# Performance work log

Measured on AMD Instinct MI355X. Metric: run time of the kernel, lower is better.

The kernel has to match this reference:

```python
import jax, jax.numpy as jnp
import numpy as np

ITEM_NUM = 100000
H = 128          # hidden_size
L_PROTO = 500    # number of prototypes
K = 4            # top-k prototypes
SEQ = 50         # max_seq_length
B = 1024
TAO = 0.1
LAMBDA = 0.1
EPS = 1e-5


def layer_norm(x, g, b):
    mu = jnp.mean(x, axis=-1, keepdims=True)
    var = jnp.mean((x - mu) ** 2, axis=-1, keepdims=True)
    return (x - mu) * jax.lax.rsqrt(var + EPS) * g + b


def setup_inputs() -> dict:
    key = jax.random.key(0)
    ks = jax.random.split(key, 12)
    std = 0.02
    item_emb = jax.random.normal(ks[0], (ITEM_NUM, H), jnp.float32) * std
    item_emb = item_emb.at[0].set(0.0)  # padding_idx=0
    pos_emb = jax.random.normal(ks[1], (SEQ + 1, H), jnp.float32) * std
    pos_emb = pos_emb.at[0].set(0.0)    # padding_idx=0 (never hit when len==SEQ)
    proto = jax.random.normal(ks[2], (L_PROTO, H), jnp.float32) * std
    w1 = jax.random.normal(ks[3], (H, H), jnp.float32) * std
    w2 = jax.random.normal(ks[4], (H, 1), jnp.float32) * std
    w3 = jax.random.normal(ks[5], (H, H), jnp.float32) * std
    w4 = jax.random.normal(ks[6], (H, H), jnp.float32) * std
    w5 = jax.random.normal(ks[7], (H, K), jnp.float32) * std
    w6 = jax.random.normal(ks[8], (H, H), jnp.float32) * std
    w7 = jax.random.normal(ks[9], (H, 1), jnp.float32) * std
    seq = jax.random.randint(ks[10], (B, SEQ), 0, ITEM_NUM, dtype=jnp.int64)
    g = jnp.ones((H,), jnp.float32)
    b = jnp.zeros((H,), jnp.float32)
    return {
        'item_emb': item_emb, 'pos_emb': pos_emb, 'proto': proto,
        'w1': w1, 'w2': w2, 'w3': w3, 'w4': w4, 'w5': w5, 'w6': w6, 'w7': w7,
        'ln1_g': g, 'ln1_b': b, 'ln2_g': g, 'ln2_b': b,
        'ln3_g': g, 'ln3_b': b, 'ln4_g': g, 'ln4_b': b,
        'seq': seq,
    }


def reference(item_emb, pos_emb, proto, w1, w2, w3, w4, w5, w6, w7,
              ln1_g, ln1_b, ln2_g, ln2_b, ln3_g, ln3_b, ln4_g, ln4_b, seq):
    mask = (seq != 0).astype(jnp.float32)            # [B,S]
    ie = item_emb[seq]                               # [B,S,H]

    # self-attentive virtual concept vector
    sa_score = jnp.squeeze(jnp.tanh(ie @ w1) @ w2, -1)   # [B,S]
    sa_score = sa_score - (1.0 - mask) * 10000.0
    alpha = jax.nn.softmax(sa_score, axis=-1)
    vcv = jnp.einsum('bs,bsh->bh', alpha, ie)            # [B,H]

    # prototype routing: top-k by score
    s = vcv @ proto.T                                    # [B,L]
    chosen_s, rank = jax.lax.top_k(s, K)                 # [B,K]
    chosen_proto = proto[rank]                           # [B,K,H]
    chosen_proto = jax.nn.sigmoid(chosen_s)[..., None] * chosen_proto

    # item->prototype assignment
    p_kt_score = jnp.einsum('bsh,bkh->bsk',
                            layer_norm(ie @ w3, ln1_g, ln1_b),
                            layer_norm(chosen_proto, ln2_g, ln2_b))
    p_kt = jax.nn.softmax(p_kt_score, axis=-1) * mask[:, :, None]  # [B,S,K]

    # positional embedding (positions SEQ..1)
    position = SEQ - jnp.arange(SEQ)                     # [S]
    emb = pos_emb[position][None, :, :] + ie             # [B,S,H]

    a_k_score = jnp.swapaxes(jnp.tanh(emb @ w4) @ w5, 1, 2)   # [B,K,S]
    a_k = jax.nn.softmax(a_k_score, axis=-1) * mask[:, None, :]
    a_k = jnp.swapaxes(a_k, 1, 2)                        # [B,S,K]

    p = p_kt * a_k
    interesting = layer_norm(jnp.einsum('bsk,bsh->bkh', p, emb), ln3_g, ln3_b)  # [B,K,H]

    xu = jnp.einsum('bsk,bkh->bsh', p_kt, chosen_proto)  # [B,S,H]
    c_score = jnp.squeeze(jnp.tanh(xu @ w6) @ w7, -1) - (1.0 - mask) * 10000.0
    c_w = jax.nn.softmax(c_score, axis=-1)               # [B,S]
    c_apt = layer_norm(jnp.einsum('bs,bsh->bh', c_w, xu), ln4_g, ln4_b)  # [B,H]

    e_score = jnp.einsum('bh,bkh->bk', c_apt, interesting)
    e = jax.nn.softmax(e_score / TAO, axis=-1)
    final = jnp.einsum('bk,bkh->bh', e, interesting)     # [B,H]
    scores = final @ item_emb.T                          # [B,ITEM_NUM]

    # prototype covariance regularizer
    centered = proto - jnp.mean(proto, axis=0, keepdims=True)
    M = (centered @ centered.T) / H
    Lc = (jnp.linalg.norm(M) - jnp.linalg.norm(jnp.diag(M))) * 0.5
    return scores, LAMBDA * Lc
```

## Files before the change

kernel.cpp:

```cpp
#include <hip/hip_runtime.h>
#include <hip/hip_bf16.h>

#define H 128
#define H2 132
#define SQL 50
#define LPROTO 500
#define KTOP 4
#define BQ 1024
#define ITEMS 100000

typedef __attribute__((ext_vector_type(8))) short bf16x8;
typedef __attribute__((ext_vector_type(4))) float f32x4;

__device__ __forceinline__ float wsum(float v){
#pragma unroll
  for (int o = 32; o; o >>= 1) v += __shfl_xor(v, o, 64);
  return v;
}
__device__ __forceinline__ float wmax(float v){
#pragma unroll
  for (int o = 32; o; o >>= 1) v = fmaxf(v, __shfl_xor(v, o, 64));
  return v;
}
__device__ __forceinline__ unsigned short f2bf(float x){
  unsigned int u = __builtin_bit_cast(unsigned int, x);
  unsigned int r = u + 0x7fffu + ((u >> 16) & 1u);
  return (unsigned short)(r >> 16);
}
__device__ __forceinline__ float bf2f(unsigned short h){
  unsigned int u = ((unsigned int)h) << 16;
  return __builtin_bit_cast(float, u);
}

__device__ __forceinline__ void mm_mfma(const float (*src)[H2], float (*dst)[H2],
                                        const unsigned short* __restrict__ wt_hi,
                                        const unsigned short* __restrict__ wt_lo,
                                        int lane, int wave)
{
  const int r15 = lane & 15;
  const int g   = lane >> 4;
  const int kof = g * 8;
  const int row = wave * 16 + r15;
  const int srow = (row < SQL) ? row : 0;

  bf16x8 ah[4], al[4];
#pragma unroll
  for (int ks = 0; ks < 4; ks++){
    const float* p = &src[srow][ks * 32 + kof];
    float4 x0 = *reinterpret_cast<const float4*>(p);
    float4 x1 = *reinterpret_cast<const float4*>(p + 4);
    float xs[8] = {x0.x, x0.y, x0.z, x0.w, x1.x, x1.y, x1.z, x1.w};
    bf16x8 h, l;
#pragma unroll
    for (int e = 0; e < 8; e++){
      unsigned short hb = f2bf(xs[e]);
      float rem = xs[e] - bf2f(hb);
      h[e] = (short)hb;
      l[e] = (short)f2bf(rem);
    }
    ah[ks] = h; al[ks] = l;
  }

  f32x4 acc[8];
#pragma unroll
  for (int j = 0; j < 8; j++) acc[j] = (f32x4){0.f, 0.f, 0.f, 0.f};

#pragma unroll
  for (int j = 0; j < 8; j++){
    const unsigned short* bp = wt_hi + (j * 16 + r15) * H + kof;
    const unsigned short* lp = wt_lo + (j * 16 + r15) * H + kof;
    f32x4 a = acc[j];
#pragma unroll
    for (int ks = 0; ks < 4; ks++){
      bf16x8 bh = *reinterpret_cast<const bf16x8*>(bp + ks * 32);
      bf16x8 bl = *reinterpret_cast<const bf16x8*>(lp + ks * 32);
      a = __builtin_amdgcn_mfma_f32_16x16x32_bf16(ah[ks], bh, a, 0, 0, 0);
      a = __builtin_amdgcn_mfma_f32_16x16x32_bf16(al[ks], bh, a, 0, 0, 0);
      a = __builtin_amdgcn_mfma_f32_16x16x32_bf16(ah[ks], bl, a, 0, 0, 0);
    }
    acc[j] = a;
  }

#pragma unroll
  for (int j = 0; j < 8; j++){
#pragma unroll
    for (int r = 0; r < 4; r++){
      int orow = wave * 16 + g * 4 + r;
      if (orow < SQL) dst[orow][j * 16 + r15] = acc[j][r];
    }
  }
}

extern "C" __global__ __launch_bounds__(256)
void sine_row(const float* __restrict__ item_emb, const float* __restrict__ pos_emb,
              const float* __restrict__ proto,
              const float* __restrict__ w2, const float* __restrict__ w5,
              const float* __restrict__ w7,
              const unsigned short* __restrict__ wt,
              const float* __restrict__ ln1g, const float* __restrict__ ln1b,
              const float* __restrict__ ln2g, const float* __restrict__ ln2b,
              const float* __restrict__ ln3g, const float* __restrict__ ln3b,
              const float* __restrict__ ln4g, const float* __restrict__ ln4b,
              const int* __restrict__ seq,
              unsigned short* __restrict__ finalbf)
{
  __shared__ __align__(16) float sA[SQL][H2];
  __shared__ __align__(16) float sE[SQL][H2];
  __shared__ __align__(16) float scp[KTOP][H];
  __shared__ __align__(16) float slncp[KTOP][H];
  __shared__ __align__(16) float sintr[KTOP][H];
  __shared__ __align__(16) float svcv[H];
  __shared__ __align__(16) float scapt[H];
  __shared__ float srow[SQL];
  __shared__ float smask[SQL];
  __shared__ float spkt[SQL][KTOP];
  __shared__ float sak[SQL][KTOP];
  __shared__ float ssc[LPROTO];
  __shared__ float schs[KTOP];
  __shared__ int   srank[KTOP];
  __shared__ float sesc[KTOP];

  const int b = blockIdx.x;
  const int t = threadIdx.x;
  const int lane = t & 63;
  const int wave = t >> 6;
  const int* sq = seq + b * SQL;

  const unsigned short* w1t_hi = wt;
  const unsigned short* w1t_lo = wt + 16384;
  const unsigned short* w3t_hi = wt + 32768;
  const unsigned short* w3t_lo = wt + 49152;
  const unsigned short* w4t_hi = wt + 65536;
  const unsigned short* w4t_lo = wt + 81920;
  const unsigned short* w6t_hi = wt + 98304;
  const unsigned short* w6t_lo = wt + 114688;

  if (t < SQL) smask[t] = (sq[t] != 0) ? 1.0f : 0.0f;
  for (int c = t; c < SQL * (H / 4); c += 256){
    int s = c >> 5, q = c & 31;
    int idx = sq[s];
    float4 v = reinterpret_cast<const float4*>(item_emb)[idx * (H / 4) + q];
    reinterpret_cast<float4*>(&sA[s][0])[q] = v;
  }
  __syncthreads();

  mm_mfma(sA, sE, w1t_hi, w1t_lo, lane, wave);
  __syncthreads();
  for (int s = wave; s < SQL; s += 4){
    float y0 = sE[s][lane], y1 = sE[s][64 + lane];
    float part = tanhf(y0) * w2[lane] + tanhf(y1) * w2[64 + lane];
    float sc = wsum(part);
    if (lane == 0) srow[s] = sc - (1.0f - smask[s]) * 10000.0f;
  }
  __syncthreads();

  if (wave == 0){
    float v = (lane < SQL) ? srow[lane] : -1e30f;
    float m = wmax(v);
    float e = (lane < SQL) ? expf(v - m) : 0.0f;
    float sum = wsum(e);
    if (lane < SQL) srow[lane] = e / sum;
  }
  __syncthreads();
  if (t < H){
    float acc = 0.f;
    for (int s = 0; s < SQL; s++) acc = fmaf(srow[s], sA[s][t], acc);
    svcv[t] = acc;
  }
  __syncthreads();

  for (int l = t; l < LPROTO; l += 256){
    const float4* pr = reinterpret_cast<const float4*>(proto + l * H);
    const float4* vc = reinterpret_cast<const float4*>(svcv);
    float acc = 0.f;
    for (int q = 0; q < H / 4; q++){
      float4 p = pr[q], v = vc[q];
      acc += p.x * v.x + p.y * v.y + p.z * v.z + p.w * v.w;
    }
    ssc[l] = acc;
  }
  __syncthreads();
  if (wave == 0){
    float cand[8];
#pragma unroll
    for (int i = 0; i < 8; i++){
      int l = lane + 64 * i;
      cand[i] = (l < LPROTO) ? ssc[l] : -1e30f;
    }
    for (int k = 0; k < KTOP; k++){
      float bv = -1e30f; int bi = 0x7fffffff;
#pragma unroll
      for (int i = 0; i < 8; i++){
        int l = lane + 64 * i;
        if (cand[i] > bv || (cand[i] == bv && l < bi)){ bv = cand[i]; bi = l; }
      }
#pragma unroll
      for (int o = 32; o; o >>= 1){
        float ov = __shfl_xor(bv, o, 64);
        int   oi = __shfl_xor(bi, o, 64);
        if (ov > bv || (ov == bv && oi < bi)){ bv = ov; bi = oi; }
      }
      if (lane == 0){ schs[k] = bv; srank[k] = bi; }
      int li = bi - lane;
#pragma unroll
      for (int i = 0; i < 8; i++) if (64 * i == li) cand[i] = -1e30f;
    }
  }
  __syncthreads();
  {
    int k = wave;
    int r = srank[k];
    float sg = 1.0f / (1.0f + expf(-schs[k]));
    float v0 = sg * proto[r * H + lane];
    float v1 = sg * proto[r * H + 64 + lane];
    float mu = wsum(v0 + v1) * (1.0f / H);
    float d0 = v0 - mu, d1 = v1 - mu;
    float var = wsum(d0 * d0 + d1 * d1) * (1.0f / H);
    float rs = rsqrtf(var + 1e-5f);
    scp[k][lane] = v0; scp[k][64 + lane] = v1;
    slncp[k][lane]      = d0 * rs * ln2g[lane]      + ln2b[lane];
    slncp[k][64 + lane] = d1 * rs * ln2g[64 + lane] + ln2b[64 + lane];
  }
  __syncthreads();

  mm_mfma(sA, sE, w3t_hi, w3t_lo, lane, wave);
  __syncthreads();
  for (int s = wave; s < SQL; s += 4){
    float a0 = sE[s][lane], a1 = sE[s][64 + lane];
    float mu = wsum(a0 + a1) * (1.0f / H);
    float d0 = a0 - mu, d1 = a1 - mu;
    float var = wsum(d0 * d0 + d1 * d1) * (1.0f / H);
    float rs = rsqrtf(var + 1e-5f);
    float l0 = d0 * rs * ln1g[lane]      + ln1b[lane];
    float l1 = d1 * rs * ln1g[64 + lane] + ln1b[64 + lane];
    float sc0 = wsum(l0 * slncp[0][lane] + l1 * slncp[0][64 + lane]);
    float sc1 = wsum(l0 * slncp[1][lane] + l1 * slncp[1][64 + lane]);
    float sc2 = wsum(l0 * slncp[2][lane] + l1 * slncp[2][64 + lane]);
    float sc3 = wsum(l0 * slncp[3][lane] + l1 * slncp[3][64 + lane]);
    float m = fmaxf(fmaxf(sc0, sc1), fmaxf(sc2, sc3));
    float e0 = expf(sc0 - m), e1 = expf(sc1 - m), e2 = expf(sc2 - m), e3 = expf(sc3 - m);
    float inv = 1.0f / (e0 + e1 + e2 + e3);
    float msk = smask[s];
    if (lane == 0){
      spkt[s][0] = e0 * inv * msk; spkt[s][1] = e1 * inv * msk;
      spkt[s][2] = e2 * inv * msk; spkt[s][3] = e3 * inv * msk;
    }
  }
  __syncthreads();

  for (int c = t; c < SQL * (H / 4); c += 256){
    int s = c >> 5, q = c & 31;
    float4 pv = reinterpret_cast<const float4*>(pos_emb + (SQL - s) * H)[q];
    float4 iv = reinterpret_cast<float4*>(&sA[s][0])[q];
    float4 r; r.x = pv.x + iv.x; r.y = pv.y + iv.y; r.z = pv.z + iv.z; r.w = pv.w + iv.w;
    reinterpret_cast<float4*>(&sE[s][0])[q] = r;
  }
  __syncthreads();

  mm_mfma(sE, sA, w4t_hi, w4t_lo, lane, wave);
  __syncthreads();
  for (int s = wave; s < SQL; s += 4){
    float t0 = tanhf(sA[s][lane]), t1 = tanhf(sA[s][64 + lane]);
    float s0 = wsum(t0 * w5[lane * 4 + 0] + t1 * w5[(64 + lane) * 4 + 0]);
    float s1 = wsum(t0 * w5[lane * 4 + 1] + t1 * w5[(64 + lane) * 4 + 1]);
    float s2 = wsum(t0 * w5[lane * 4 + 2] + t1 * w5[(64 + lane) * 4 + 2]);
    float s3 = wsum(t0 * w5[lane * 4 + 3] + t1 * w5[(64 + lane) * 4 + 3]);
    if (lane == 0){ sak[s][0] = s0; sak[s][1] = s1; sak[s][2] = s2; sak[s][3] = s3; }
  }
  __syncthreads();

  {
    int k = wave;
    float v = (lane < SQL) ? sak[lane][k] : -1e30f;
    float m = wmax(v);
    float e = (lane < SQL) ? expf(v - m) : 0.0f;
    float sum = wsum(e);
    if (lane < SQL) sak[lane][k] = (e / sum) * smask[lane] * spkt[lane][k];
  }
  __syncthreads();

  for (int c = t; c < KTOP * H; c += 256){
    int k = c >> 7, h = c & 127;
    float acc = 0.f;
    for (int s = 0; s < SQL; s++) acc = fmaf(sak[s][k], sE[s][h], acc);
    sintr[k][h] = acc;
  }
  __syncthreads();
  {
    int k = wave;
    float v0 = sintr[k][lane], v1 = sintr[k][64 + lane];
    float mu = wsum(v0 + v1) * (1.0f / H);
    float d0 = v0 - mu, d1 = v1 - mu;
    float var = wsum(d0 * d0 + d1 * d1) * (1.0f / H);
    float rs = rsqrtf(var + 1e-5f);
    sintr[k][lane]      = d0 * rs * ln3g[lane]      + ln3b[lane];
    sintr[k][64 + lane] = d1 * rs * ln3g[64 + lane] + ln3b[64 + lane];
  }
  __syncthreads();

  for (int c = t; c < SQL * H; c += 256){
    int s = c >> 7, h = c & 127;
    float acc = spkt[s][0] * scp[0][h] + spkt[s][1] * scp[1][h]
              + spkt[s][2] * scp[2][h] + spkt[s][3] * scp[3][h];
    sA[s][h] = acc;
  }
  __syncthreads();
  mm_mfma(sA, sE, w6t_hi, w6t_lo, lane, wave);
  __syncthreads();
  for (int s = wave; s < SQL; s += 4){
    float part = tanhf(sE[s][lane]) * w7[lane] + tanhf(sE[s][64 + lane]) * w7[64 + lane];
    float sc = wsum(part);
    if (lane == 0) srow[s] = sc - (1.0f - smask[s]) * 10000.0f;
  }
  __syncthreads();

  if (wave == 0){
    float v = (lane < SQL) ? srow[lane] : -1e30f;
    float m = wmax(v);
    float e = (lane < SQL) ? expf(v - m) : 0.0f;
    float sum = wsum(e);
    if (lane < SQL) srow[lane] = e / sum;
  }
  __syncthreads();
  if (t < H){
    float acc = 0.f;
    for (int s = 0; s < SQL; s++) acc = fmaf(srow[s], sA[s][t], acc);
    scapt[t] = acc;
  }
  __syncthreads();
  if (wave == 0){
    float v0 = scapt[lane], v1 = scapt[64 + lane];
    float mu = wsum(v0 + v1) * (1.0f / H);
    float d0 = v0 - mu, d1 = v1 - mu;
    float var = wsum(d0 * d0 + d1 * d1) * (1.0f / H);
    float rs = rsqrtf(var + 1e-5f);
    scapt[lane]      = d0 * rs * ln4g[lane]      + ln4b[lane];
    scapt[64 + lane] = d1 * rs * ln4g[64 + lane] + ln4b[64 + lane];
  }
  __syncthreads();

  {
    int k = wave;
    float part = scapt[lane] * sintr[k][lane] + scapt[64 + lane] * sintr[k][64 + lane];
    float sc = wsum(part);
    if (lane == 0) sesc[k] = sc;
  }
  __syncthreads();
  if (t < H){
    float e0 = sesc[0] * 10.0f, e1 = sesc[1] * 10.0f, e2 = sesc[2] * 10.0f, e3 = sesc[3] * 10.0f;
    float m = fmaxf(fmaxf(e0, e1), fmaxf(e2, e3));
    float x0 = expf(e0 - m), x1 = expf(e1 - m), x2 = expf(e2 - m), x3 = expf(e3 - m);
    float inv = 1.0f / (x0 + x1 + x2 + x3);
    float f = (x0 * sintr[0][t] + x1 * sintr[1][t] + x2 * sintr[2][t] + x3 * sintr[3][t]) * inv;
    finalbf[b * H + t] = f2bf(f);
  }
}

extern "C" __global__ void wprep(const float* __restrict__ w1, const float* __restrict__ w3,
                                 const float* __restrict__ w4, const float* __restrict__ w6,
                                 unsigned short* __restrict__ out){
  const float* srcs[4] = {w1, w3, w4, w6};
  const float* src = srcs[blockIdx.x];
  unsigned short* hi = out + blockIdx.x * 32768;
  unsigned short* lo = hi + 16384;
  for (int i = threadIdx.x; i < 16384; i += 256){
    int c = i >> 7, k = i & 127;
    float f = src[k * H + c];
    unsigned short h = f2bf(f);
    hi[i] = h;
    lo[i] = f2bf(f - bf2f(h));
  }
}

extern "C" __global__ void conv_bf16(const float* __restrict__ in,
                                     unsigned short* __restrict__ out, int n4){
  int i = blockIdx.x * blockDim.x + threadIdx.x;
  int stride = gridDim.x * blockDim.x;
  for (; i < n4; i += stride){
    float4 v = reinterpret_cast<const float4*>(in)[i];
    union { unsigned short u[4]; uint2 v2; } o;
    o.u[0] = f2bf(v.x); o.u[1] = f2bf(v.y); o.u[2] = f2bf(v.z); o.u[3] = f2bf(v.w);
    reinterpret_cast<uint2*>(out)[i] = o.v2;
  }
}

#define GBM 64
#define GBN 128
#define LDT 136

extern "C" __global__ __launch_bounds__(256)
void gemm_scores(const unsigned short* __restrict__ A,
                 const unsigned short* __restrict__ Bm,
                 float* __restrict__ C)
{
  __shared__ __align__(16) unsigned short sA[GBM][LDT];
  __shared__ __align__(16) unsigned short sB[GBN][LDT];
  const int t = threadIdx.x, lane = t & 63, wave = t >> 6;
  const int n0 = blockIdx.x * GBN;
  const int m0 = blockIdx.y * GBM;

  for (int c = t; c < GBM * 16; c += 256){
    int r = c >> 4, q = c & 15;
    uint4 v = reinterpret_cast<const uint4*>(A + (m0 + r) * H)[q];
    *reinterpret_cast<uint4*>(&sA[r][q * 8]) = v;
  }
  for (int c = t; c < GBN * 16; c += 256){
    int r = c >> 4, q = c & 15;
    int n = n0 + r;
    uint4 v = make_uint4(0u, 0u, 0u, 0u);
    if (n < ITEMS) v = reinterpret_cast<const uint4*>(Bm + n * H)[q];
    *reinterpret_cast<uint4*>(&sB[r][q * 8]) = v;
  }
  __syncthreads();

  const int wm = wave >> 1, wn = wave & 1;
  f32x4 acc[2][4];
#pragma unroll
  for (int i = 0; i < 2; i++)
#pragma unroll
    for (int j = 0; j < 4; j++) acc[i][j] = (f32x4){0.f, 0.f, 0.f, 0.f};

#pragma unroll
  for (int ks = 0; ks < 4; ks++){
    bf16x8 af[2], bfr[4];
#pragma unroll
    for (int i = 0; i < 2; i++)
      af[i] = *reinterpret_cast<const bf16x8*>(&sA[wm * 32 + i * 16 + (lane & 15)][ks * 32 + (lane >> 4) * 8]);
#pragma unroll
    for (int j = 0; j < 4; j++)
      bfr[j] = *reinterpret_cast<const bf16x8*>(&sB[wn * 64 + j * 16 + (lane & 15)][ks * 32 + (lane >> 4) * 8]);
#pragma unroll
    for (int i = 0; i < 2; i++)
#pragma unroll
      for (int j = 0; j < 4; j++)
        acc[i][j] = __builtin_amdgcn_mfma_f32_16x16x32_bf16(af[i], bfr[j], acc[i][j], 0, 0, 0);
  }

#pragma unroll
  for (int i = 0; i < 2; i++){
    int mrow = m0 + wm * 32 + i * 16 + (lane >> 4) * 4;
#pragma unroll
    for (int j = 0; j < 4; j++){
      int ncol = n0 + wn * 64 + j * 16 + (lane & 15);
      if (ncol < ITEMS){
#pragma unroll
        for (int r = 0; r < 4; r++)
          C[(size_t)(mrow + r) * ITEMS + ncol] = acc[i][j][r];
      }
    }
  }
}

extern "C" __global__ void proto_mean(const float* __restrict__ proto,
                                      float* __restrict__ mean, float* __restrict__ accum){
  int h = threadIdx.x;
  if (h < 2) accum[h] = 0.0f;
  float acc = 0.f;
  for (int l = 0; l < LPROTO; l++) acc += proto[l * H + h];
  mean[h] = acc * (1.0f / LPROTO);
}

extern "C" __global__ __launch_bounds__(256)
void proto_cov(const float* __restrict__ proto, const float* __restrict__ mean,
               float* __restrict__ accum){
  __shared__ float ci[H];
  __shared__ float red[256];
  int i = blockIdx.x, t = threadIdx.x;
  if (t < H) ci[t] = proto[i * H + t] - mean[t];
  __syncthreads();
  float total = 0.f;
  for (int j = t; j < LPROTO; j += 256){
    float acc = 0.f;
    for (int h = 0; h < H; h++) acc = fmaf(ci[h], proto[j * H + h] - mean[h], acc);
    float m = acc * (1.0f / H);
    total += m * m;
    if (j == i) atomicAdd(&accum[1], m * m);
  }
  red[t] = total; __syncthreads();
  for (int o = 128; o; o >>= 1){ if (t < o) red[t] += red[t + o]; __syncthreads(); }
  if (t == 0) atomicAdd(&accum[0], red[0]);
}

extern "C" __global__ void lc_final(const float* __restrict__ accum, float* __restrict__ out){
  out[(size_t)BQ * ITEMS] = 0.1f * 0.5f * (sqrtf(accum[0]) - sqrtf(accum[1]));
}

extern "C" void kernel_launch(void* const* d_in, const int* in_sizes, int n_in,
                              void* d_out, int out_size, void* d_ws, size_t ws_size,
                              hipStream_t stream){
  const float* item  = (const float*)d_in[0];
  const float* pos   = (const float*)d_in[1];
  const float* proto = (const float*)d_in[2];
  const float* w1 = (const float*)d_in[3];
  const float* w2 = (const float*)d_in[4];
  const float* w3 = (const float*)d_in[5];
  const float* w4 = (const float*)d_in[6];
  const float* w5 = (const float*)d_in[7];
  const float* w6 = (const float*)d_in[8];
  const float* w7 = (const float*)d_in[9];
  const float* ln1g = (const float*)d_in[10];
  const float* ln1b = (const float*)d_in[11];
  const float* ln2g = (const float*)d_in[12];
  const float* ln2b = (const float*)d_in[13];
  const float* ln3g = (const float*)d_in[14];
  const float* ln3b = (const float*)d_in[15];
  const float* ln4g = (const float*)d_in[16];
  const float* ln4b = (const float*)d_in[17];
  const int* seq = (const int*)d_in[18];
  float* out = (float*)d_out;

  char* ws = (char*)d_ws;
  float* accum = (float*)ws;
  float* mean  = (float*)(ws + 256);
  unsigned short* finalbf = (unsigned short*)(ws + 1024);
  unsigned short* itembf  = (unsigned short*)(ws + 263168);
  unsigned short* wtbuf   = (unsigned short*)(ws + 25863168);

  wprep<<<4, 256, 0, stream>>>(w1, w3, w4, w6, wtbuf);
  conv_bf16<<<2048, 256, 0, stream>>>(item, itembf, ITEMS * H / 4);

  sine_row<<<BQ, 256, 0, stream>>>(item, pos, proto, w2, w5, w7, wtbuf,
                                   ln1g, ln1b, ln2g, ln2b, ln3g, ln3b, ln4g, ln4b,
                                   seq, finalbf);

  gemm_scores<<<dim3((ITEMS + GBN - 1) / GBN, BQ / GBM), 256, 0, stream>>>(finalbf, itembf, out);

  proto_mean<<<1, 128, 0, stream>>>(proto, mean, accum);
  proto_cov<<<LPROTO, 256, 0, stream>>>(proto, mean, accum);
  lc_final<<<1, 1, 0, stream>>>(accum, out);
}
```

Measured before the change: 429.7 us.

## Fuse MFMA epilogues into register reductions and enlarge score GEMM M-tile

The per-row kernel now keeps the four projection matmul results in MFMA accumulator registers. It computes the tanh/weight dot products, the layernorm and the routing scores directly from those registers using 16-lane shuffle reductions, so it no longer writes the results to shared memory and rereads them behind an extra barrier. Separately, the scores GEMM tile grows from 64 to 128 rows per block, which halves the number of blocks and raises reuse of each item-embedding tile. The larger tile and extra accumulators raise register and LDS use per block, which may lower occupancy.

Measured after the change: 378.9 us. -11.8%, faster.

```diff
diff --git a/kernel.cpp b/kernel.cpp
--- a/kernel.cpp
+++ b/kernel.cpp
@@ -22,6 +22,13 @@
   for (int o = 32; o; o >>= 1) v = fmaxf(v, __shfl_xor(v, o, 64));
   return v;
 }
+__device__ __forceinline__ float gr16(float v){
+  v += __shfl_xor(v, 1, 64);
+  v += __shfl_xor(v, 2, 64);
+  v += __shfl_xor(v, 4, 64);
+  v += __shfl_xor(v, 8, 64);
+  return v;
+}
 __device__ __forceinline__ unsigned short f2bf(float x){
   unsigned int u = __builtin_bit_cast(unsigned int, x);
   unsigned int r = u + 0x7fffu + ((u >> 16) & 1u);
@@ -32,21 +39,21 @@
   return __builtin_bit_cast(float, u);
 }
 
-__device__ __forceinline__ void mm_mfma(const float (*src)[H2], float (*dst)[H2],
-                                        const unsigned short* __restrict__ wt_hi,
-                                        const unsigned short* __restrict__ wt_lo,
-                                        int lane, int wave)
+__device__ __forceinline__ void mm_acc(const float (*src)[H2],
+                                       const unsigned short* __restrict__ wt_hi,
+                                       const unsigned short* __restrict__ wt_lo,
+                                       int lane, int wave, f32x4* acc)
 {
   const int r15 = lane & 15;
   const int g   = lane >> 4;
   const int kof = g * 8;
   const int row = wave * 16 + r15;
-  const int srow = (row < SQL) ? row : 0;
+  const int srw = (row < SQL) ? row : 0;
 
   bf16x8 ah[4], al[4];
 #pragma unroll
   for (int ks = 0; ks < 4; ks++){
-    const float* p = &src[srow][ks * 32 + kof];
+    const float* p = &src[srw][ks * 32 + kof];
     float4 x0 = *reinterpret_cast<const float4*>(p);
     float4 x1 = *reinterpret_cast<const float4*>(p + 4);
     float xs[8] = {x0.x, x0.y, x0.z, x0.w, x1.x, x1.y, x1.z, x1.w};
@@ -61,12 +68,9 @@
     ah[ks] = h; al[ks] = l;
   }
 
-  f32x4 acc[8];
-#pragma unroll
-  for (int j = 0; j < 8; j++) acc[j] = (f32x4){0.f, 0.f, 0.f, 0.f};
-
 #pragma unroll
   for (int j = 0; j < 8; j++){
+    acc[j] = (f32x4){0.f, 0.f, 0.f, 0.f};
     const unsigned short* bp = wt_hi + (j * 16 + r15) * H + kof;
     const unsigned short* lp = wt_lo + (j * 16 + r15) * H + kof;
     f32x4 a = acc[j];
@@ -79,15 +83,6 @@
       a = __builtin_amdgcn_mfma_f32_16x16x32_bf16(ah[ks], bl, a, 0, 0, 0);
     }
     acc[j] = a;
-  }
-
-#pragma unroll
-  for (int j = 0; j < 8; j++){
-#pragma unroll
-    for (int r = 0; r < 4; r++){
-      int orow = wave * 16 + g * 4 + r;
-      if (orow < SQL) dst[orow][j * 16 + r15] = acc[j][r];
-    }
   }
 }
 
@@ -124,6 +119,8 @@
   const int t = threadIdx.x;
   const int lane = t & 63;
   const int wave = t >> 6;
+  const int r15 = lane & 15;
+  const int g   = lane >> 4;
   const int* sq = seq + b * SQL;
 
   const unsigned short* w1t_hi = wt;
@@ -144,13 +141,27 @@
   }
   __syncthreads();
 
-  mm_mfma(sA, sE, w1t_hi, w1t_lo, lane, wave);
-  __syncthreads();
-  for (int s = wave; s < SQL; s += 4){
-    float y0 = sE[s][lane], y1 = sE[s][64 + lane];
-    float part = tanhf(y0) * w2[lane] + tanhf(y1) * w2[64 + lane];
-    float sc = wsum(part);
-    if (lane == 0) srow[s] = sc - (1.0f - smask[s]) * 10000.0f;
+  {
+    f32x4 acc[8];
+    mm_acc(sA, w1t_hi, w1t_lo, lane, wave, acc);
+    float p0 = 0.f, p1 = 0.f, p2 = 0.f, p3 = 0.f;
+#pragma unroll
+    for (int j = 0; j < 8; j++){
+      float w2c = w2[j * 16 + r15];
+      p0 = fmaf(tanhf(acc[j][0]), w2c, p0);
+      p1 = fmaf(tanhf(acc[j][1]), w2c, p1);
+      p2 = fmaf(tanhf(acc[j][2]), w2c, p2);
+      p3 = fmaf(tanhf(acc[j][3]), w2c, p3);
+    }
+    p0 = gr16(p0); p1 = gr16(p1); p2 = gr16(p2); p3 = gr16(p3);
+    if (r15 == 0){
+      float pv[4] = {p0, p1, p2, p3};
+#pragma unroll
+      for (int r = 0; r < 4; r++){
+        int orow = wave * 16 + g * 4 + r;
+        if (orow < SQL) srow[orow] = pv[r] - (1.0f - smask[orow]) * 10000.0f;
+      }
+    }
   }
   __syncthreads();
 
@@ -223,31 +234,68 @@
   }
   __syncthreads();
 
-  mm_mfma(sA, sE, w3t_hi, w3t_lo, lane, wave);
-  __syncthreads();
-  for (int s = wave; s < SQL; s += 4){
-    float a0 = sE[s][lane], a1 = sE[s][64 + lane];
-    float mu = wsum(a0 + a1) * (1.0f / H);
-    float d0 = a0 - mu, d1 = a1 - mu;
-    float var = wsum(d0 * d0 + d1 * d1) * (1.0f / H);
-    float rs = rsqrtf(var + 1e-5f);
-    float l0 = d0 * rs * ln1g[lane]      + ln1b[lane];
-    float l1 = d1 * rs * ln1g[64 + lane] + ln1b[64 + lane];
-    float sc0 = wsum(l0 * slncp[0][lane] + l1 * slncp[0][64 + lane]);
-    float sc1 = wsum(l0 * slncp[1][lane] + l1 * slncp[1][64 + lane]);
-    float sc2 = wsum(l0 * slncp[2][lane] + l1 * slncp[2][64 + lane]);
-    float sc3 = wsum(l0 * slncp[3][lane] + l1 * slncp[3][64 + lane]);
-    float m = fmaxf(fmaxf(sc0, sc1), fmaxf(sc2, sc3));
-    float e0 = expf(sc0 - m), e1 = expf(sc1 - m), e2 = expf(sc2 - m), e3 = expf(sc3 - m);
-    float inv = 1.0f / (e0 + e1 + e2 + e3);
-    float msk = smask[s];
-    if (lane == 0){
-      spkt[s][0] = e0 * inv * msk; spkt[s][1] = e1 * inv * msk;
-      spkt[s][2] = e2 * inv * msk; spkt[s][3] = e3 * inv * msk;
-    }
-  }
-  __syncthreads();
-
+  {
+    f32x4 acc[8];
+    mm_acc(sA, w3t_hi, w3t_lo, lane, wave, acc);
+    float s0 = 0.f, s1 = 0.f, s2 = 0.f, s3 = 0.f;
+#pragma unroll
+    for (int j = 0; j < 8; j++){ s0 += acc[j][0]; s1 += acc[j][1]; s2 += acc[j][2]; s3 += acc[j][3]; }
+    float mu0 = gr16(s0) * (1.0f / H), mu1 = gr16(s1) * (1.0f / H);
+    float mu2 = gr16(s2) * (1.0f / H), mu3 = gr16(s3) * (1.0f / H);
+    float q0 = 0.f, q1 = 0.f, q2 = 0.f, q3 = 0.f;
+#pragma unroll
+    for (int j = 0; j < 8; j++){
+      float d0 = acc[j][0] - mu0, d1 = acc[j][1] - mu1;
+      float d2 = acc[j][2] - mu2, d3 = acc[j][3] - mu3;
+      q0 = fmaf(d0, d0, q0); q1 = fmaf(d1, d1, q1);
+      q2 = fmaf(d2, d2, q2); q3 = fmaf(d3, d3, q3);
+    }
+    float rs0 = rsqrtf(gr16(q0) * (1.0f / H) + 1e-5f);
+    float rs1 = rsqrtf(gr16(q1) * (1.0f / H) + 1e-5f);
+    float rs2 = rsqrtf(gr16(q2) * (1.0f / H) + 1e-5f);
+    float rs3 = rsqrtf(gr16(q3) * (1.0f / H) + 1e-5f);
+    float pk[4][4];
+#pragma unroll
+    for (int k = 0; k < 4; k++)
+#pragma unroll
+      for (int r = 0; r < 4; r++) pk[k][r] = 0.f;
+#pragma unroll
+    for (int j = 0; j < 8; j++){
+      int c = j * 16 + r15;
+      float gg = ln1g[c], bb = ln1b[c];
+      float l0 = fmaf((acc[j][0] - mu0) * rs0, gg, bb);
+      float l1 = fmaf((acc[j][1] - mu1) * rs1, gg, bb);
+      float l2 = fmaf((acc[j][2] - mu2) * rs2, gg, bb);
+      float l3 = fmaf((acc[j][3] - mu3) * rs3, gg, bb);
+#pragma unroll
+      for (int k = 0; k < 4; k++){
+        float w = slncp[k][c];
+        pk[k][0] = fmaf(l0, w, pk[k][0]);
+        pk[k][1] = fmaf(l1, w, pk[k][1]);
+        pk[k][2] = fmaf(l2, w, pk[k][2]);
+        pk[k][3] = fmaf(l3, w, pk[k][3]);
+      }
+    }
+#pragma unroll
+    for (int k = 0; k < 4; k++)
+#pragma unroll
+      for (int r = 0; r < 4; r++) pk[k][r] = gr16(pk[k][r]);
+    if (r15 == 0){
+#pragma unroll
+      for (int r = 0; r < 4; r++){
+        int orow = wave * 16 + g * 4 + r;
+        if (orow < SQL){
+          float m = fmaxf(fmaxf(pk[0][r], pk[1][r]), fmaxf(pk[2][r], pk[3][r]));
+          float e0 = expf(pk[0][r] - m), e1 = expf(pk[1][r] - m);
+          float e2 = expf(pk[2][r] - m), e3 = expf(pk[3][r] - m);
+          float inv = 1.0f / (e0 + e1 + e2 + e3);
+          float msk = smask[orow];
+          spkt[orow][0] = e0 * inv * msk; spkt[orow][1] = e1 * inv * msk;
+          spkt[orow][2] = e2 * inv * msk; spkt[orow][3] = e3 * inv * msk;
+        }
+      }
+    }
+  }
   for (int c = t; c < SQL * (H / 4); c += 256){
     int s = c >> 5, q = c & 31;
     float4 pv = reinterpret_cast<const float4*>(pos_emb + (SQL - s) * H)[q];
@@ -257,15 +305,43 @@
   }
   __syncthreads();
 
-  mm_mfma(sE, sA, w4t_hi, w4t_lo, lane, wave);
-  __syncthreads();
-  for (int s = wave; s < SQL; s += 4){
-    float t0 = tanhf(sA[s][lane]), t1 = tanhf(sA[s][64 + lane]);
-    float s0 = wsum(t0 * w5[lane * 4 + 0] + t1 * w5[(64 + lane) * 4 + 0]);
-    float s1 = wsum(t0 * w5[lane * 4 + 1] + t1 * w5[(64 + lane) * 4 + 1]);
-    float s2 = wsum(t0 * w5[lane * 4 + 2] + t1 * w5[(64 + lane) * 4 + 2]);
-    float s3 = wsum(t0 * w5[lane * 4 + 3] + t1 * w5[(64 + lane) * 4 + 3]);
-    if (lane == 0){ sak[s][0] = s0; sak[s][1] = s1; sak[s][2] = s2; sak[s][3] = s3; }
+  {
+    f32x4 acc[8];
+    mm_acc(sE, w4t_hi, w4t_lo, lane, wave, acc);
+    float pk[4][4];
+#pragma unroll
+    for (int k = 0; k < 4; k++)
+#pragma unroll
+      for (int r = 0; r < 4; r++) pk[k][r] = 0.f;
+#pragma unroll
+    for (int j = 0; j < 8; j++){
+      int c = j * 16 + r15;
+      float4 w5c = *reinterpret_cast<const float4*>(w5 + c * 4);
+      float t0 = tanhf(acc[j][0]), t1 = tanhf(acc[j][1]);
+      float t2 = tanhf(acc[j][2]), t3 = tanhf(acc[j][3]);
+      pk[0][0] = fmaf(t0, w5c.x, pk[0][0]); pk[0][1] = fmaf(t1, w5c.x, pk[0][1]);
+      pk[0][2] = fmaf(t2, w5c.x, pk[0][2]); pk[0][3] = fmaf(t3, w5c.x, pk[0][3]);
+      pk[1][0] = fmaf(t0, w5c.y, pk[1][0]); pk[1][1] = fmaf(t1, w5c.y, pk[1][1]);
+      pk[1][2] = fmaf(t2, w5c.y, pk[1][2]); pk[1][3] = fmaf(t3, w5c.y, pk[1][3]);
+      pk[2][0] = fmaf(t0, w5c.z, pk[2][0]); pk[2][1] = fmaf(t1, w5c.z, pk[2][1]);
+      pk[2][2] = fmaf(t2, w5c.z, pk[2][2]); pk[2][3] = fmaf(t3, w5c.z, pk[2][3]);
+      pk[3][0] = fmaf(t0, w5c.w, pk[3][0]); pk[3][1] = fmaf(t1, w5c.w, pk[3][1]);
+      pk[3][2] = fmaf(t2, w5c.w, pk[3][2]); pk[3][3] = fmaf(t3, w5c.w, pk[3][3]);
+    }
+#pragma unroll
+    for (int k = 0; k < 4; k++)
+#pragma unroll
+      for (int r = 0; r < 4; r++) pk[k][r] = gr16(pk[k][r]);
+    if (r15 == 0){
+#pragma unroll
+      for (int r = 0; r < 4; r++){
+        int orow = wave * 16 + g * 4 + r;
+        if (orow < SQL){
+          sak[orow][0] = pk[0][r]; sak[orow][1] = pk[1][r];
+          sak[orow][2] = pk[2][r]; sak[orow][3] = pk[3][r];
+        }
+      }
+    }
   }
   __syncthreads();
 
@@ -305,12 +381,27 @@
     sA[s][h] = acc;
   }
   __syncthreads();
-  mm_mfma(sA, sE, w6t_hi, w6t_lo, lane, wave);
-  __syncthreads();
-  for (int s = wave; s < SQL; s += 4){
-    float part = tanhf(sE[s][lane]) * w7[lane] + tanhf(sE[s][64 + lane]) * w7[64 + lane];
-    float sc = wsum(part);
-    if (lane == 0) srow[s] = sc - (1.0f - smask[s]) * 10000.0f;
+  {
+    f32x4 acc[8];
+    mm_acc(sA, w6t_hi, w6t_lo, lane, wave, acc);
+    float p0 = 0.f, p1 = 0.f, p2 = 0.f, p3 = 0.f;
+#pragma unroll
+    for (int j = 0; j < 8; j++){
+      float w7c = w7[j * 16 + r15];
+      p0 = fmaf(tanhf(acc[j][0]), w7c, p0);
+      p1 = fmaf(tanhf(acc[j][1]), w7c, p1);
+      p2 = fmaf(tanhf(acc[j][2]), w7c, p2);
+      p3 = fmaf(tanhf(acc[j][3]), w7c, p3);
+    }
+    p0 = gr16(p0); p1 = gr16(p1); p2 = gr16(p2); p3 = gr16(p3);
+    if (r15 == 0){
+      float pv[4] = {p0, p1, p2, p3};
+#pragma unroll
+      for (int r = 0; r < 4; r++){
+        int orow = wave * 16 + g * 4 + r;
+        if (orow < SQL) srow[orow] = pv[r] - (1.0f - smask[orow]) * 10000.0f;
+      }
+    }
   }
   __syncthreads();
 
@@ -384,7 +475,7 @@
   }
 }
 
-#define GBM 64
+#define GBM 128
 #define GBN 128
 #define LDT 136
 
@@ -396,6 +487,7 @@
   __shared__ __align__(16) unsigned short sA[GBM][LDT];
   __shared__ __align__(16) unsigned short sB[GBN][LDT];
   const int t = threadIdx.x, lane = t & 63, wave = t >> 6;
+  const int r15 = lane & 15, g = lane >> 4;
   const int n0 = blockIdx.x * GBN;
   const int m0 = blockIdx.y * GBM;
 
@@ -408,40 +500,40 @@
     int r = c >> 4, q = c & 15;
     int n = n0 + r;
     uint4 v = make_uint4(0u, 0u, 0u, 0u);
-    if (n < ITEMS) v = reinterpret_cast<const uint4*>(Bm + n * H)[q];
+    if (n < ITEMS) v = reinterpret_cast<const uint4*>(Bm + (size_t)n * H)[q];
     *reinterpret_cast<uint4*>(&sB[r][q * 8]) = v;
   }
   __syncthreads();
 
   const int wm = wave >> 1, wn = wave & 1;
-  f32x4 acc[2][4];
-#pragma unroll
-  for (int i = 0; i < 2; i++)
+  f32x4 acc[4][4];
+#pragma unroll
+  for (int i = 0; i < 4; i++)
 #pragma unroll
     for (int j = 0; j < 4; j++) acc[i][j] = (f32x4){0.f, 0.f, 0.f, 0.f};
 
 #pragma unroll
   for (int ks = 0; ks < 4; ks++){
-    bf16x8 af[2], bfr[4];
-#pragma unroll
-    for (int i = 0; i < 2; i++)
-      af[i] = *reinterpret_cast<const bf16x8*>(&sA[wm * 32 + i * 16 + (lane & 15)][ks * 32 + (lane >> 4) * 8]);
+    bf16x8 af[4], bfr[4];
+#pragma unroll
+    for (int i = 0; i < 4; i++)
+      af[i] = *reinterpret_cast<const bf16x8*>(&sA[wm * 64 + i * 16 + r15][ks * 32 + g * 8]);
 #pragma unroll
     for (int j = 0; j < 4; j++)
-      bfr[j] = *reinterpret_cast<const bf16x8*>(&sB[wn * 64 + j * 16 + (lane & 15)][ks * 32 + (lane >> 4) * 8]);
-#pragma unroll
-    for (int i = 0; i < 2; i++)
+      bfr[j] = *reinterpret_cast<const bf16x8*>(&sB[wn * 64 + j * 16 + r15][ks * 32 + g * 8]);
+#pragma unroll
+    for (int i = 0; i < 4; i++)
 #pragma unroll
       for (int j = 0; j < 4; j++)
         acc[i][j] = __builtin_amdgcn_mfma_f32_16x16x32_bf16(af[i], bfr[j], acc[i][j], 0, 0, 0);
   }
 
 #pragma unroll
-  for (int i = 0; i < 2; i++){
-    int mrow = m0 + wm * 32 + i * 16 + (lane >> 4) * 4;
+  for (int i = 0; i < 4; i++){
+    int mrow = m0 + wm * 64 + i * 16 + g * 4;
 #pragma unroll
     for (int j = 0; j < 4; j++){
-      int ncol = n0 + wn * 64 + j * 16 + (lane & 15);
+      int ncol = n0 + wn * 64 + j * 16 + r15;
       if (ncol < ITEMS){
 #pragma unroll
         for (int r = 0; r < 4; r++)
```
